# Performance work log

Measured on AMD Instinct MI355X. Metric: run time of the kernel, lower is better.

Reference implementation:

```python
import jax, jax.numpy as jnp
import numpy as np
import math

B, C, H, W = 8, 384, 14, 14
HEADS = 12
HC = C // HEADS
STRIDE = 2
K = 3
FACTOR = 2.0
rH = -(-H // STRIDE)
rW = -(-W // STRIDE)
N = H * W
S = rH * rW
KK = K * K
OFFSET_MAT = np.array([[0, -1], [-1, -1], [-1, 0], [-1, 1], [0, 1], [1, 1], [1, 0], [1, -1], [0, 0]], dtype=np.float32)


def bilinear_sample(img, coords):
    """img (Hi,Wi,C); coords (...,2) normalized (y,x) in [-1,1].
    Matches F.grid_sample(mode='bilinear', align_corners=True, padding_mode='zeros')."""
    Hi, Wi = img.shape[0], img.shape[1]
    py = (coords[..., 0] + 1.0) * 0.5 * (Hi - 1)
    px = (coords[..., 1] + 1.0) * 0.5 * (Wi - 1)
    y0 = jnp.floor(py)
    x0 = jnp.floor(px)
    wy1 = py - y0
    wx1 = px - x0

    def corner(yf, xf, wgt):
        valid = (yf >= 0) & (yf <= Hi - 1) & (xf >= 0) & (xf <= Wi - 1)
        yi = jnp.clip(yf, 0, Hi - 1).astype(jnp.int32)
        xi = jnp.clip(xf, 0, Wi - 1).astype(jnp.int32)
        return img[yi, xi] * (wgt * valid)[..., None]

    return (corner(y0, x0, (1 - wy1) * (1 - wx1)) + corner(y0, x0 + 1, (1 - wy1) * wx1)
            + corner(y0 + 1, x0, wy1 * (1 - wx1)) + corner(y0 + 1, x0 + 1, wy1 * wx1))


def _forward(x, Wq, bq, Wk, bk, Wv, bv, Wo1, bo1, Wdw, bdw, ln_g, ln_b, Wo2, Wco, posembed, Wp, bp):
    dt = x.dtype
    xh = jnp.transpose(x, (0, 2, 3, 1))                       # B,H,W,C
    q = jnp.einsum('bhwc,oc->bhwo', xh, Wq) + bq              # q_conv (1x1)

    # ---- offset network: 1x1 conv -> GELU -> 3x3 dw stride conv -> LN -> GELU -> 1x1 ----
    t = jax.nn.gelu(jnp.einsum('bhwc,oc->bhwo', q, Wo1) + bo1, approximate=False)
    ker = jnp.transpose(Wdw, (2, 3, 1, 0))                    # (3,3,1,C) for HWIO depthwise
    t = jax.lax.conv_general_dilated(t, ker, (STRIDE, STRIDE), ((1, 1), (1, 1)),
                                     dimension_numbers=('NHWC', 'HWIO', 'NHWC'),
                                     feature_group_count=C) + bdw  # B,rH,rW,C
    mu = t.mean(-1, keepdims=True)
    var = ((t - mu) ** 2).mean(-1, keepdims=True)
    t = (t - mu) / jnp.sqrt(var + 1e-5) * ln_g + ln_b
    t = jax.nn.gelu(t, approximate=False)
    off = jnp.einsum('bhwc,oc->bhwo', t, Wo2)                 # B,rH,rW,2*N ; channel = (g,h,w)
    off = off.reshape(B, rH, rW, 2, N)
    off = jnp.transpose(off, (0, 3, 4, 1, 2))                 # B,2,N,rH,rW
    ranges = jnp.array([1.0 / H, 1.0 / W], dtype=dt)
    off = jnp.tanh(off) * ranges[None, :, None, None, None] * FACTOR
    off = jnp.transpose(off, (0, 2, 3, 4, 1))                 # B,N,rH,rW,2 (y,x)

    # ---- strided reference grid + deformable bilinear gather from x ----
    gy = jnp.arange(0, H, STRIDE, dtype=dt) / (H - 1) * 2 - 1
    gx = jnp.arange(0, W, STRIDE, dtype=dt) / (W - 1) * 2 - 1
    ref = jnp.stack(jnp.meshgrid(gy, gx, indexing='ij'), -1)  # rH,rW,2
    dpos = off + ref
    sampled = jax.vmap(bilinear_sample)(xh, dpos).reshape(B, N, S, C)

    # ---- k x k center points with learned offsets ----
    cy = jnp.arange(H, dtype=dt)
    cx = jnp.arange(W, dtype=dt)
    center = jnp.stack(jnp.meshgrid(cy, cx, indexing='ij'), -1).reshape(N, 1, 2)
    offmat = jnp.asarray(OFFSET_MAT, dtype=dt)
    cpt = center + offmat[None]                               # N,KK,2
    cpt_norm = jnp.stack([jnp.clip(cpt[..., 0], 0, H) / (H - 1) * 2 - 1,
                          jnp.clip(cpt[..., 1], 0, W) / (W - 1) * 2 - 1], -1).reshape(N, K, K, 2)
    q_tok = q.reshape(B, N, C)
    co = jnp.tanh(jnp.einsum('bnc,oc->bno', q_tok, Wco).reshape(B, N, K, K, 2)) * ranges
    cgrid = co + cpt_norm[None]
    csampled = jax.vmap(bilinear_sample)(xh, cgrid).reshape(B, N, KK, C)

    feats = jnp.concatenate([sampled, csampled], axis=2)      # B,N,S+KK,C
    k = (jnp.einsum('bnsc,oc->bnso', feats, Wk) + bk).reshape(B, N, S + KK, HEADS, HC)
    v = (jnp.einsum('bnsc,oc->bnso', feats, Wv) + bv).reshape(B, N, S + KK, HEADS, HC)
    qh = q_tok.reshape(B, N, HEADS, HC)
    attn = jnp.einsum('bnhd,bnshd->bhns', qh, k)              # qk_scale=None -> no scaling

    # ---- dynamic relative position bias (grid_sample into rel-pos table) ----
    a = jnp.arange(0, H, STRIDE, dtype=dt)
    bcol = jnp.arange(0, W, dtype=dt)
    ref_pos = a[None, :] - bcol[:, None]                      # (W, rH)
    ref_pos_x = jnp.tile(ref_pos, (H, rH))                    # (N, S)
    ref_pos_y = jnp.repeat(jnp.repeat(ref_pos, W, axis=0), rW, axis=1)
    rpp = jnp.stack([ref_pos_y / (H - 1), ref_pos_x / (W - 1)], -1)  # N,S,2
    rel = rpp.reshape(N, rH, rW, 2)[None] - off               # B,N,rH,rW,2
    table = jnp.transpose(posembed, (1, 2, 0))                # (2H-1, 2W-1, heads)
    d_rel = bilinear_sample(table, rel).reshape(B, N, S, HEADS)
    cpt_raw = jnp.broadcast_to(center, (N, KK, 2)).reshape(N, K, K, 2)
    crel = co - cpt_raw[None]
    d_crel = bilinear_sample(table, crel).reshape(B, N, KK, HEADS)
    bias = jnp.concatenate([d_rel, d_crel], axis=2)           # B,N,S+KK,heads
    attn = attn + jnp.transpose(bias, (0, 3, 1, 2))
    attn = jax.nn.softmax(attn, axis=-1)

    out = jnp.einsum('bhns,bnshd->bnhd', attn, v).reshape(B, N, C)
    out = jnp.einsum('bnc,oc->bno', out, Wp) + bp             # proj (1x1)
    return jnp.transpose(out.reshape(B, H, W, C), (0, 3, 1, 2))


def setup_inputs() -> dict:
    key = jax.random.key(0)
    ks = jax.random.split(key, 20)
    def w(k, shape, s=0.05):
        return jax.random.normal(k, shape, dtype=jnp.float32) * s
    return {
        'x': jax.random.normal(ks[0], (B, C, H, W), dtype=jnp.float32),
        'Wq': w(ks[1], (C, C)), 'bq': w(ks[2], (C,)),
        'Wk': w(ks[3], (C, C)), 'bk': w(ks[4], (C,)),
        'Wv': w(ks[5], (C, C)), 'bv': w(ks[6], (C,)),
        'Wo1': w(ks[7], (C, C)), 'bo1': w(ks[8], (C,)),
        'Wdw': w(ks[9], (C, 1, 3, 3), 0.2), 'bdw': w(ks[10], (C,)),
        'ln_g': jnp.ones((C,), jnp.float32), 'ln_b': jnp.zeros((C,), jnp.float32),
        'Wo2': w(ks[11], (2 * N, C)),
        'Wco': w(ks[12], (2 * K * K, C)),
        'posembed': w(ks[13], (HEADS, 2 * H - 1, 2 * W - 1), 0.02),
        'Wp': w(ks[14], (C, C)), 'bp': w(ks[15], (C,)),
    }


def reference(x, Wq, bq, Wk, bk, Wv, bv, Wo1, bo1, Wdw, bdw, ln_g, ln_b, Wo2, Wco, posembed, Wp, bp):
    return _forward(x, Wq, bq, Wk, bk, Wv, bv, Wo1, bo1, Wdw, bdw, ln_g, ln_b, Wo2, Wco, posembed, Wp, bp)
```

## Files before the change

### kernel.cpp

```cpp
#include <hip/hip_runtime.h>
#include <hip/hip_bf16.h>
#include <math.h>

#define BB 8
#define CC 384
#define HH 14
#define WW 14
#define NHEADS 12
#define RH 7
#define RW 7
#define NN 196
#define SS 49
#define KKK 9
#define SK 58
#define TH 27
#define NTOK 1568

typedef float    f4 __attribute__((ext_vector_type(4)));
typedef _Float16 h8 __attribute__((ext_vector_type(8)));
typedef _Float16 h4 __attribute__((ext_vector_type(4)));

__device__ __forceinline__ float geluf(float x){ return 0.5f*x*(1.0f+erff(x*0.7071067811865475f)); }
__device__ __forceinline__ f4 mfma16h(h8 a, h8 b, f4 c){
  return __builtin_amdgcn_mfma_f32_16x16x32_f16(a, b, c, 0, 0, 0);
}

__constant__ float c_offm[9][2] = {{0,-1},{-1,-1},{-1,0},{-1,1},{0,1},{1,1},{1,0},{1,-1},{0,0}};

__global__ void __launch_bounds__(256) k_transpose2(const float* __restrict__ x,
                                                    float* __restrict__ xh, _Float16* __restrict__ xhh){
  __shared__ float tile[48*203];
  int b = blockIdx.x >> 3, c0 = (blockIdx.x & 7)*48;
  int t = threadIdx.x;
  for (int i = t; i < 48*49; i += 256){
    int row = i / 49, seg = i % 49;
    f4 v = *(const f4*)(x + ((size_t)(b*CC + c0 + row))*NN + seg*4);
    #pragma unroll
    for (int j = 0; j < 4; ++j) tile[row*203 + seg*4 + j] = v[j];
  }
  __syncthreads();
  for (int i = t; i < 196*12; i += 256){
    int n = i / 12, seg = i % 12;
    f4 v; h4 vh;
    #pragma unroll
    for (int j = 0; j < 4; ++j){ v[j] = tile[(seg*4 + j)*203 + n]; vh[j] = (_Float16)v[j]; }
    size_t o = ((size_t)(b*NN + n))*CC + c0 + seg*4;
    *(f4*)(xh + o) = v;
    *(h4*)(xhh + o) = vh;
  }
}

__device__ __forceinline__ void gemm_hilo_body(
    const float* __restrict__ A, const float* __restrict__ W,
    int arow, int brow, _Float16* sbuf, int t, f4 acc[4]){
  _Float16* Ah = sbuf; _Float16* Al = sbuf + 2560;
  _Float16* Bh = sbuf + 5120; _Float16* Bl = sbuf + 7680;
  int w = t>>6, lane = t&63, col = lane&15, quad = lane>>4;
  int r = t>>2, cg = t&3;
  const float* Ar = A + (size_t)arow*384 + cg*8;
  const float* Br = W + (size_t)brow*384 + cg*8;
  f4 a0 = *(const f4*)(Ar),     a1 = *(const f4*)(Ar + 4);
  f4 b0 = *(const f4*)(Br),     b1 = *(const f4*)(Br + 4);
  for (int k0 = 0; k0 < 384; k0 += 32){
    h8 ah, al, bh, bl;
    #pragma unroll
    for (int j = 0; j < 4; ++j){
      ah[j] = (_Float16)a0[j];   al[j] = (_Float16)(a0[j] - (float)ah[j]);
      ah[4+j] = (_Float16)a1[j]; al[4+j] = (_Float16)(a1[j] - (float)ah[4+j]);
      bh[j] = (_Float16)b0[j];   bl[j] = (_Float16)(b0[j] - (float)bh[j]);
      bh[4+j] = (_Float16)b1[j]; bl[4+j] = (_Float16)(b1[j] - (float)bh[4+j]);
    }
    __syncthreads();
    *(h8*)(Ah + r*40 + cg*8) = ah; *(h8*)(Al + r*40 + cg*8) = al;
    *(h8*)(Bh + r*40 + cg*8) = bh; *(h8*)(Bl + r*40 + cg*8) = bl;
    __syncthreads();
    if (k0 < 352){
      a0 = *(const f4*)(Ar + k0 + 32); a1 = *(const f4*)(Ar + k0 + 36);
      b0 = *(const f4*)(Br + k0 + 32); b1 = *(const f4*)(Br + k0 + 36);
    }
    h8 afh = *(const h8*)(Ah + (w*16+col)*40 + quad*8);
    h8 afl = *(const h8*)(Al + (w*16+col)*40 + quad*8);
    #pragma unroll
    for (int nt = 0; nt < 4; ++nt){
      h8 bfh = *(const h8*)(Bh + (nt*16+col)*40 + quad*8);
      h8 bfl = *(const h8*)(Bl + (nt*16+col)*40 + quad*8);
      acc[nt] = mfma16h(afh, bfh, acc[nt]);
      acc[nt] = mfma16h(afl, bfh, acc[nt]);
      acc[nt] = mfma16h(afh, bfl, acc[nt]);
    }
  }
}

template<int EPI>
__global__ void __launch_bounds__(256) k_mmf(const float* __restrict__ A, const float* __restrict__ W,
                                             const float* __restrict__ bias, float* __restrict__ out,
                                             _Float16* __restrict__ out16, int M, int N){
  __shared__ __align__(16) _Float16 sbuf[10240];
  int t = threadIdx.x;
  int w = t>>6, lane = t&63, col = lane&15, quad = lane>>4;
  int m0 = blockIdx.x*64, n0 = blockIdx.y*64;
  int r = t>>2;
  int arow = min(m0 + r, M-1);
  int brow = min(n0 + r, N-1);
  f4 acc[4] = {{0,0,0,0},{0,0,0,0},{0,0,0,0},{0,0,0,0}};
  gemm_hilo_body(A, W, arow, brow, sbuf, t, acc);
  if constexpr (EPI == 2){
    float* tile = (float*)sbuf;
    __syncthreads();
    #pragma unroll
    for (int nt = 0; nt < 4; ++nt)
      #pragma unroll
      for (int rr = 0; rr < 4; ++rr)
        tile[(w*16 + quad*4 + rr)*65 + nt*16 + col] = acc[nt][rr];
    __syncthreads();
    for (int i = t; i < 1024; i += 256){
      int o_l = i >> 4, ms = i & 15;
      int m = m0 + ms*4;
      if (m >= M) continue;
      int bb = m / NN, nnn = m % NN;
      int o = n0 + o_l;
      float bo = bias[o];
      f4 v = { tile[(ms*4+0)*65 + o_l] + bo, tile[(ms*4+1)*65 + o_l] + bo,
               tile[(ms*4+2)*65 + o_l] + bo, tile[(ms*4+3)*65 + o_l] + bo };
      *(f4*)(out + ((size_t)bb*384 + o)*NN + nnn) = v;
    }
  } else {
    #pragma unroll
    for (int nt = 0; nt < 4; ++nt){
      #pragma unroll
      for (int rr = 0; rr < 4; ++rr){
        int m = m0 + w*16 + quad*4 + rr;
        int o = n0 + nt*16 + col;
        if (m >= M || o >= N) continue;
        float v = acc[nt][rr] + bias[o];
        if (EPI == 1) v = geluf(v);
        out[(size_t)m*384 + o] = v;
      }
    }
  }
}

__global__ void __launch_bounds__(256) k_qkv(
    const float* __restrict__ xh, const _Float16* __restrict__ xhh,
    const float* __restrict__ Wq, const float* __restrict__ bq,
    const float* __restrict__ Wk, const float* __restrict__ Wv,
    float* __restrict__ qf, _Float16* __restrict__ K2h, _Float16* __restrict__ VprojT){
  __shared__ __align__(16) _Float16 sbuf[10240];
  int t = threadIdx.x;
  int w = t>>6, lane = t&63, col = lane&15, quad = lane>>4;
  int bid = blockIdx.x;

  if (bid < 300){
    int isK = (bid >= 150) ? 1 : 0;
    int r2 = isK ? bid - 150 : bid;
    const float* W = isK ? Wk : Wq;
    int m0 = (r2/6)*64, n0 = (r2%6)*64;
    int r = t>>2;
    int arow = min(m0 + r, NTOK-1);
    int brow = n0 + r;
    f4 acc[4] = {{0,0,0,0},{0,0,0,0},{0,0,0,0},{0,0,0,0}};
    gemm_hilo_body(xh, W, arow, brow, sbuf, t, acc);
    #pragma unroll
    for (int nt = 0; nt < 4; ++nt){
      #pragma unroll
      for (int rr = 0; rr < 4; ++rr){
        int m = m0 + w*16 + quad*4 + rr;
        int o = n0 + nt*16 + col;
        if (m >= NTOK) continue;
        if (isK){
          K2h[(size_t)m*384 + o] = (_Float16)acc[nt][rr];
        } else {
          qf[(size_t)m*384 + o] = acc[nt][rr] + bq[o];
        }
      }
    }
  } else {
    int idx = bid - 300;
    int mo = idx % 6;
    int ny = (idx / 6) % 4;
    int b  = idx / 24;
    int m0 = mo*64, n0 = ny*64;
    int orow = m0 + w*16 + col;
    const float* wvr = Wv + (size_t)orow*384;
    f4 acc[4] = {{0,0,0,0},{0,0,0,0},{0,0,0,0},{0,0,0,0}};
    for (int kt = 0; kt < 12; ++kt){
      f4 a0 = *(const f4*)(wvr + kt*32 + quad*8);
      f4 a1 = *(const f4*)(wvr + kt*32 + quad*8 + 4);
      h8 ah, al;
      #pragma unroll
      for (int j = 0; j < 4; ++j){
        ah[j] = (_Float16)a0[j];   al[j] = (_Float16)(a0[j] - (float)ah[j]);
        ah[4+j] = (_Float16)a1[j]; al[4+j] = (_Float16)(a1[j] - (float)ah[4+j]);
      }
      #pragma unroll
      for (int nt = 0; nt < 4; ++nt){
        int i = min(n0 + nt*16 + col, 195);
        h8 b8 = *(const h8*)(xhh + ((size_t)(b*196 + i))*384 + kt*32 + quad*8);
        acc[nt] = mfma16h(ah, b8, acc[nt]);
        acc[nt] = mfma16h(al, b8, acc[nt]);
      }
    }
    #pragma unroll
    for (int nt = 0; nt < 4; ++nt){
      #pragma unroll
      for (int rr = 0; rr < 4; ++rr){
        int o = m0 + w*16 + quad*4 + rr;
        int i = n0 + nt*16 + col;
        if (i < 224)
          VprojT[((size_t)(b*384 + o))*224 + i] = (i < 196) ? (_Float16)acc[nt][rr] : (_Float16)0.f;
      }
    }
  }
}

__global__ void __launch_bounds__(384) k_dwln(const float* __restrict__ t1,
      const float* __restrict__ Wdw, const float* __restrict__ bdw,
      const float* __restrict__ lng, const float* __restrict__ lnb,
      float* __restrict__ t2){
  int blk = blockIdx.x;
  int ow = blk % RW; int oh = (blk / RW) % RH; int b = blk / (RH*RW);
  int c = threadIdx.x;
  float acc = bdw[c];
  #pragma unroll
  for (int kh = 0; kh < 3; ++kh){
    int ih = oh*2 - 1 + kh;
    if (ih < 0 || ih >= HH) continue;
    #pragma unroll
    for (int kw = 0; kw < 3; ++kw){
      int iw = ow*2 - 1 + kw;
      if (iw < 0 || iw >= WW) continue;
      acc += t1[((b*HH + ih)*WW + iw)*CC + c] * Wdw[c*9 + kh*3 + kw];
    }
  }
  __shared__ float red[6];
  __shared__ float s_mu, s_rv;
  float v = acc;
  #pragma unroll
  for (int o = 32; o > 0; o >>= 1) v += __shfl_down(v, o);
  int wid = c >> 6, lane = c & 63;
  if (lane == 0) red[wid] = v;
  __syncthreads();
  if (c == 0){ float s = 0.f; for (int i = 0; i < 6; ++i) s += red[i]; s_mu = s / CC; }
  __syncthreads();
  float mu = s_mu;
  float d = acc - mu;
  v = d*d;
  #pragma unroll
  for (int o = 32; o > 0; o >>= 1) v += __shfl_down(v, o);
  if (lane == 0) red[wid] = v;
  __syncthreads();
  if (c == 0){ float s = 0.f; for (int i = 0; i < 6; ++i) s += red[i]; s_rv = rsqrtf(s / CC + 1e-5f); }
  __syncthreads();
  float val = d * s_rv * lng[c] + lnb[c];
  t2[blk*CC + c] = geluf(val);
}

__global__ void __launch_bounds__(256) k_off(const float* __restrict__ t2, const float* __restrict__ Wo2,
                                             float* __restrict__ offp){
  __shared__ __align__(16) _Float16 sbuf[10240];
  int t = threadIdx.x;
  int w = t>>6, lane = t&63, col = lane&15, quad = lane>>4;
  int bid = blockIdx.x;
  int m0 = (bid/7)*64, n0 = (bid%7)*64;
  int r = t>>2;
  int arow = min(m0 + r, 391);
  int brow = min(n0 + r, 391);
  f4 acc[4] = {{0,0,0,0},{0,0,0,0},{0,0,0,0},{0,0,0,0}};
  gemm_hilo_body(t2, Wo2, arow, brow, sbuf, t, acc);
  #pragma unroll
  for (int nt = 0; nt < 4; ++nt){
    #pragma unroll
    for (int rr = 0; rr < 4; ++rr){
      int row = m0 + w*16 + quad*4 + rr;
      int o = n0 + nt*16 + col;
      if (row < 392 && o < 392){
        int g = o / NN, nn = o % NN;
        int b = row / SS, s = row % SS;
        float rng = (g == 0) ? (1.0f/HH) : (1.0f/WW);
        offp[((b*NN + nn)*SS + s)*2 + g] = tanhf(acc[nt][rr]) * rng * 2.0f;
      }
    }
  }
}

__global__ void __launch_bounds__(256, 7) k_fused(
    const float* __restrict__ qf, const float* __restrict__ off,
    const _Float16* __restrict__ K2h,
    const float* __restrict__ bk, const float* __restrict__ Wco, const float* __restrict__ pos,
    _Float16* __restrict__ agg16){
  __shared__ __align__(16) _Float16 Gs[2352];
  __shared__ __align__(16) _Float16 qh16[384];
  __shared__ __align__(16) float agg[12*228];
  __shared__ float scoreS[696];
  __shared__ float offl[98];
  __shared__ float colb[18];
  __shared__ float qbv[12];
  __shared__ uint2 tapv[232];
  float* qrow = agg;

  int blk = blockIdx.x;
  int n = blk % NN, b = blk / NN;
  int iy = n / WW, ix = n % WW;
  int t = threadIdx.x;

  {
    const f4* q4 = (const f4*)(qf + (size_t)blk*384);
    for (int i = t; i < 96; i += 256){
      f4 v = q4[i];
      ((f4*)qrow)[i] = v;
      h4 vh;
      #pragma unroll
      for (int j = 0; j < 4; ++j) vh[j] = (_Float16)v[j];
      *(h4*)(qh16 + i*4) = vh;
    }
  }
  for (int i = t; i < 98; i += 256) offl[i] = off[(size_t)blk*98 + i];
  __syncthreads();

  if (t < NN){
    const _Float16* kr = K2h + ((size_t)(b*NN + t))*384;
    for (int h = 0; h < NHEADS; ++h){
      float acc = 0.f;
      #pragma unroll
      for (int c = 0; c < 4; ++c){
        h8 kv = *(const h8*)(kr + h*32 + c*8);
        h8 qv = *(const h8*)(qh16 + h*32 + c*8);
        #pragma unroll
        for (int j = 0; j < 8; ++j) acc += (float)qv[j] * (float)kv[j];
      }
      Gs[h*NN + t] = (_Float16)acc;
    }
  }
  __syncthreads();

  if (t < 144){
    int o = t >> 3, l = t & 7;
    const float* wr = Wco + o*384 + l*48;
    const float* qr = qrow + l*48;
    f4 a4 = {0.f,0.f,0.f,0.f};
    #pragma unroll
    for (int c = 0; c < 48; c += 4) a4 += (*(const f4*)(qr + c)) * (*(const f4*)(wr + c));
    float acc = a4[0]+a4[1]+a4[2]+a4[3];
    acc += __shfl_xor(acc, 1); acc += __shfl_xor(acc, 2); acc += __shfl_xor(acc, 4);
    if (l == 0){
      int g = o & 1;
      float range = (g == 0) ? (1.0f/HH) : (1.0f/WW);
      colb[o] = tanhf(acc) * range;
    }
  }
  if (t >= 160){
    int o = t - 160;
    int h = o >> 3, l = o & 7;
    float acc = 0.f;
    for (int d = l; d < 32; d += 8) acc += qrow[h*32 + d] * bk[h*32 + d];
    acc += __shfl_xor(acc, 1); acc += __shfl_xor(acc, 2); acc += __shfl_xor(acc, 4);
    if (l == 0 && h < 12) qbv[h] = acc;
  }
  __syncthreads();

  if (t < SK){
    float cy, cx;
    if (t < SS){
      int sy = t / RW, sx = t % RW;
      cy = offl[t*2+0] + ((2.0f*sy)/13.0f*2.0f - 1.0f);
      cx = offl[t*2+1] + ((2.0f*sx)/13.0f*2.0f - 1.0f);
    } else {
      int kk = t - SS;
      float cyr = fminf(fmaxf((float)iy + c_offm[kk][0], 0.f), (float)HH);
      float cxr = fminf(fmaxf((float)ix + c_offm[kk][1], 0.f), (float)WW);
      cy = colb[kk*2+0] + (cyr/13.0f*2.0f - 1.0f);
      cx = colb[kk*2+1] + (cxr/13.0f*2.0f - 1.0f);
    }
    float py = (cy + 1.0f)*0.5f*13.0f;
    float px = (cx + 1.0f)*0.5f*13.0f;
    float y0 = floorf(py), x0 = floorf(px);
    float wy1 = py - y0, wx1 = px - x0;
    #pragma unroll
    for (int k4 = 0; k4 < 4; ++k4){
      float yf = y0 + (k4 >> 1), xf = x0 + (k4 & 1);
      bool valid = (yf >= 0.f) && (yf <= 13.f) && (xf >= 0.f) && (xf <= 13.f);
      int yi = (int)fminf(fmaxf(yf, 0.f), 13.f);
      int xi = (int)fminf(fmaxf(xf, 0.f), 13.f);
      float wgt = ((k4 >> 1) ? wy1 : (1.f - wy1)) * ((k4 & 1) ? wx1 : (1.f - wx1));
      tapv[t*4 + k4] = make_uint2(__float_as_uint(valid ? wgt : 0.f),
                                  (unsigned)(yi*WW + xi));
    }
  }
  __syncthreads();
  for (int i = t; i < 12*228; i += 256) agg[i] = 0.f;

  for (int i = t; i < SK*NHEADS; i += 256){
    int s = i / NHEADS, h = i - s*NHEADS;
    float ry, rx;
    if (s < SS){
      int sy = s / RW, sx = s % RW;
      ry = (2.0f*sy - iy)/13.0f - offl[s*2+0];
      rx = (2.0f*sx - ix)/13.0f - offl[s*2+1];
    } else {
      int kk = s - SS;
      ry = colb[kk*2+0] - (float)iy;
      rx = colb[kk*2+1] - (float)ix;
    }
    float py = (ry + 1.0f)*0.5f*26.0f;
    float px = (rx + 1.0f)*0.5f*26.0f;
    float y0 = floorf(py), x0 = floorf(px);
    float wy1 = py - y0, wx1 = px - x0;
    float val = qbv[h];
    #pragma unroll
    for (int k4 = 0; k4 < 4; ++k4){
      float yf = y0 + (k4 >> 1), xf = x0 + (k4 & 1);
      if (yf >= 0.f && yf <= 26.f && xf >= 0.f && xf <= 26.f){
        int yi = (int)yf, xi = (int)xf;
        float wgt = ((k4 >> 1) ? wy1 : (1.f - wy1)) * ((k4 & 1) ? wx1 : (1.f - wx1));
        val += pos[(h*TH + yi)*TH + xi] * wgt;
      }
    }
    #pragma unroll
    for (int k4 = 0; k4 < 4; ++k4){
      uint2 tp = tapv[s*4 + k4];
      val += __uint_as_float(tp.x) * (float)Gs[h*196 + (int)tp.y];
    }
    scoreS[h*58 + s] = val;
  }
  __syncthreads();

  if (t < 192){
    int h = t >> 4, l = t & 15;
    float v[4];
    #pragma unroll
    for (int k = 0; k < 4; ++k){ int s = l + 16*k; v[k] = (s < SK) ? scoreS[h*58 + s] : -1e30f; }
    float mx = fmaxf(fmaxf(v[0], v[1]), fmaxf(v[2], v[3]));
    mx = fmaxf(mx, __shfl_xor(mx, 1)); mx = fmaxf(mx, __shfl_xor(mx, 2));
    mx = fmaxf(mx, __shfl_xor(mx, 4)); mx = fmaxf(mx, __shfl_xor(mx, 8));
    float e[4], sum = 0.f;
    #pragma unroll
    for (int k = 0; k < 4; ++k){ int s = l + 16*k; e[k] = (s < SK) ? expf(v[k] - mx) : 0.f; sum += e[k]; }
    sum += __shfl_xor(sum, 1); sum += __shfl_xor(sum, 2);
    sum += __shfl_xor(sum, 4); sum += __shfl_xor(sum, 8);
    float inv = 1.0f / sum;
    #pragma unroll
    for (int k = 0; k < 4; ++k){
      int s = l + 16*k;
      if (s < SK) scoreS[h*58 + s] = e[k]*inv;
    }
  }
  __syncthreads();

  for (int i = t; i < 232*NHEADS; i += 256){
    int tap = i / NHEADS, h = i - tap*NHEADS;
    int s = tap >> 2;
    uint2 tp = tapv[tap];
    float v = scoreS[h*58 + s] * __uint_as_float(tp.x);
    atomicAdd(&agg[h*228 + (int)tp.y], v);
  }
  __syncthreads();

  {
    _Float16* ar = agg16 + (size_t)blk*2688;
    for (int i = t; i < 336; i += 256){
      int d = i*8;
      int h = d / 224, j = d - h*224;
      const float* src = agg + h*228 + j;
      f4 a = *(const f4*)src;
      f4 c = *(const f4*)(src + 4);
      h8 o;
      #pragma unroll
      for (int k = 0; k < 4; ++k){ o[k] = (_Float16)a[k]; o[4+k] = (_Float16)c[k]; }
      *(h8*)(ar + d) = o;
    }
  }
}

__global__ void __launch_bounds__(256) k_av(const _Float16* __restrict__ agg16,
                                            const _Float16* __restrict__ VprojT,
                                            const float* __restrict__ bv, float* __restrict__ otok){
  int t = threadIdx.x;
  int w = t>>6, lane = t&63, col = lane&15, quad = lane>>4;
  int m0 = blockIdx.x*64;
  int bh = blockIdx.y; int b = bh / 12, h = bh - b*12;
  const _Float16* ar = agg16 + ((size_t)(b*196 + min(m0 + w*16 + col, 195)))*2688 + h*224;
  f4 acc[2] = {{0,0,0,0},{0,0,0,0}};
  for (int kt = 0; kt < 7; ++kt){
    h8 a8 = *(const h8*)(ar + kt*32 + quad*8);
    #pragma unroll
    for (int nt = 0; nt < 2; ++nt){
      int o = h*32 + nt*16 + col;
      h8 b8 = *(const h8*)(VprojT + ((size_t)(b*384 + o))*224 + kt*32 + quad*8);
      acc[nt] = mfma16h(a8, b8, acc[nt]);
    }
  }
  #pragma unroll
  for (int nt = 0; nt < 2; ++nt){
    #pragma unroll
    for (int rr = 0; rr < 4; ++rr){
      int m = m0 + w*16 + quad*4 + rr;
      if (m < 196){
        int o = h*32 + nt*16 + col;
        otok[((size_t)(b*196 + m))*384 + o] = acc[nt][rr] + bv[o];
      }
    }
  }
}

extern "C" void kernel_launch(void* const* d_in, const int* in_sizes, int n_in,
                              void* d_out, int out_size, void* d_ws, size_t ws_size,
                              hipStream_t stream){
  const float* x    = (const float*)d_in[0];
  const float* Wq   = (const float*)d_in[1];
  const float* bq   = (const float*)d_in[2];
  const float* Wk   = (const float*)d_in[3];
  const float* bk   = (const float*)d_in[4];
  const float* Wv   = (const float*)d_in[5];
  const float* bv   = (const float*)d_in[6];
  const float* Wo1  = (const float*)d_in[7];
  const float* bo1  = (const float*)d_in[8];
  const float* Wdw  = (const float*)d_in[9];
  const float* bdw  = (const float*)d_in[10];
  const float* ln_g = (const float*)d_in[11];
  const float* ln_b = (const float*)d_in[12];
  const float* Wo2  = (const float*)d_in[13];
  const float* Wco  = (const float*)d_in[14];
  const float* pos  = (const float*)d_in[15];
  const float* Wp   = (const float*)d_in[16];
  const float* bp   = (const float*)d_in[17];
  float* out = (float*)d_out;

  float* ws   = (float*)d_ws;
  float* xh   = ws;
  float* qf   = xh   + 602112;
  float* t1   = qf   + 602112;
  float* t2   = t1   + 602112;
  float* offp = t2   + 150528;
  float* otok = offp + 153664;
  _Float16* xhh    = (_Float16*)(otok + 602112);
  _Float16* K2h    = xhh    + 602112;
  _Float16* VprojT = K2h    + 602112;
  _Float16* agg16  = VprojT + 688128;

  k_transpose2<<<64, 256, 0, stream>>>(x, xh, xhh);
  k_qkv<<<492, 256, 0, stream>>>(xh, xhh, Wq, bq, Wk, Wv, qf, K2h, VprojT);
  k_mmf<1><<<dim3(25,6), 256, 0, stream>>>(qf, Wo1, bo1, t1, nullptr, NTOK, 384);
  k_dwln<<<392, 384, 0, stream>>>(t1, Wdw, bdw, ln_g, ln_b, t2);
  k_off<<<49, 256, 0, stream>>>(t2, Wo2, offp);
  k_fused<<<1568, 256, 0, stream>>>(qf, offp, K2h, bk, Wco, pos, agg16);
  k_av<<<dim3(4,96), 256, 0, stream>>>(agg16, VprojT, bv, otok);
  k_mmf<2><<<dim3(25,6), 256, 0, stream>>>(otok, Wp, bp, out, nullptr, NTOK, 384);
}
```

Measured before the change: 223.1 us.

## Precompute per-head Q·K^T with an MFMA kernel instead of per-block scalar dots

Adds a k_qkt kernel that computes the full per-head Q·K^T matrix (196x196 per batch-head) using 16x16x32 f16 MFMA and stores it to a global fp16 buffer. k_fused then copies its 2352-element row from global into shared memory, where before it computed the dot products with scalar fp16 loops. This swaps scalar ALU work and repeated K reads in every block for one matrix-core pass. The cost is an extra launch and a round trip of about 7 MB of fp16 scores through global memory.

```diff
diff --git a/kernel.cpp b/kernel.cpp
--- a/kernel.cpp
+++ b/kernel.cpp
@@ -283,13 +283,44 @@
   }
 }
 
+__global__ void __launch_bounds__(256) k_qkt(const float* __restrict__ qf, const _Float16* __restrict__ K2h,
+                                             _Float16* __restrict__ G16){
+  int t = threadIdx.x;
+  int w = t>>6, lane = t&63, col = lane&15, quad = lane>>4;
+  int m0 = blockIdx.x*64;
+  int bh = blockIdx.y; int b = bh / 12, h = bh - b*12;
+  const float* qr = qf + ((size_t)(b*196 + min(m0 + w*16 + col, 195)))*384 + h*32;
+  f4 q0 = *(const f4*)(qr + quad*8);
+  f4 q1 = *(const f4*)(qr + quad*8 + 4);
+  h8 a8;
+  #pragma unroll
+  for (int j = 0; j < 4; ++j){ a8[j] = (_Float16)q0[j]; a8[4+j] = (_Float16)q1[j]; }
+  f4 acc[13];
+  #pragma unroll
+  for (int nt = 0; nt < 13; ++nt){
+    int i = min(nt*16 + col, 195);
+    h8 b8 = *(const h8*)(K2h + ((size_t)(b*196 + i))*384 + h*32 + quad*8);
+    f4 z = {0.f,0.f,0.f,0.f};
+    acc[nt] = mfma16h(a8, b8, z);
+  }
+  #pragma unroll
+  for (int nt = 0; nt < 13; ++nt){
+    #pragma unroll
+    for (int r = 0; r < 4; ++r){
+      int m = m0 + w*16 + quad*4 + r;
+      int i = nt*16 + col;
+      if (m < 196 && i < 196)
+        G16[((size_t)(b*196 + m))*2352 + h*196 + i] = (_Float16)acc[nt][r];
+    }
+  }
+}
+
 __global__ void __launch_bounds__(256, 7) k_fused(
     const float* __restrict__ qf, const float* __restrict__ off,
-    const _Float16* __restrict__ K2h,
+    const _Float16* __restrict__ G16,
     const float* __restrict__ bk, const float* __restrict__ Wco, const float* __restrict__ pos,
     _Float16* __restrict__ agg16){
   __shared__ __align__(16) _Float16 Gs[2352];
-  __shared__ __align__(16) _Float16 qh16[384];
   __shared__ __align__(16) float agg[12*228];
   __shared__ float scoreS[696];
   __shared__ float offl[98];
@@ -304,33 +335,16 @@
   int t = threadIdx.x;
 
   {
+    const h8* g8 = (const h8*)(G16 + (size_t)blk*2352);
+    h8* gs8 = (h8*)Gs;
+    for (int i = t; i < 294; i += 256) gs8[i] = g8[i];
+  }
+  {
     const f4* q4 = (const f4*)(qf + (size_t)blk*384);
-    for (int i = t; i < 96; i += 256){
-      f4 v = q4[i];
-      ((f4*)qrow)[i] = v;
-      h4 vh;
-      #pragma unroll
-      for (int j = 0; j < 4; ++j) vh[j] = (_Float16)v[j];
-      *(h4*)(qh16 + i*4) = vh;
-    }
+    f4* qr4 = (f4*)qrow;
+    for (int i = t; i < 96; i += 256) qr4[i] = q4[i];
   }
   for (int i = t; i < 98; i += 256) offl[i] = off[(size_t)blk*98 + i];
-  __syncthreads();
-
-  if (t < NN){
-    const _Float16* kr = K2h + ((size_t)(b*NN + t))*384;
-    for (int h = 0; h < NHEADS; ++h){
-      float acc = 0.f;
-      #pragma unroll
-      for (int c = 0; c < 4; ++c){
-        h8 kv = *(const h8*)(kr + h*32 + c*8);
-        h8 qv = *(const h8*)(qh16 + h*32 + c*8);
-        #pragma unroll
-        for (int j = 0; j < 8; ++j) acc += (float)qv[j] * (float)kv[j];
-      }
-      Gs[h*NN + t] = (_Float16)acc;
-    }
-  }
   __syncthreads();
 
   if (t < 144){
@@ -535,14 +549,16 @@
   _Float16* xhh    = (_Float16*)(otok + 602112);
   _Float16* K2h    = xhh    + 602112;
   _Float16* VprojT = K2h    + 602112;
-  _Float16* agg16  = VprojT + 688128;
+  _Float16* G16    = VprojT + 688128;
+  _Float16* agg16  = G16    + 3687936;
 
   k_transpose2<<<64, 256, 0, stream>>>(x, xh, xhh);
   k_qkv<<<492, 256, 0, stream>>>(xh, xhh, Wq, bq, Wk, Wv, qf, K2h, VprojT);
   k_mmf<1><<<dim3(25,6), 256, 0, stream>>>(qf, Wo1, bo1, t1, nullptr, NTOK, 384);
   k_dwln<<<392, 384, 0, stream>>>(t1, Wdw, bdw, ln_g, ln_b, t2);
   k_off<<<49, 256, 0, stream>>>(t2, Wo2, offp);
-  k_fused<<<1568, 256, 0, stream>>>(qf, offp, K2h, bk, Wco, pos, agg16);
+  k_qkt<<<dim3(4,96), 256, 0, stream>>>(qf, K2h, G16);
+  k_fused<<<1568, 256, 0, stream>>>(qf, offp, G16, bk, Wco, pos, agg16);
   k_av<<<dim3(4,96), 256, 0, stream>>>(agg16, VprojT, bv, otok);
   k_mmf<2><<<dim3(25,6), 256, 0, stream>>>(otok, Wp, bp, out, nullptr, NTOK, 384);
 }
```

Result: faster. 207.8 us (-6.8%).
